# Kernel optimization log

Hardware: AMD Instinct MI355X
Metric: run time of the kernel (lower is better)

The kernel has to match this reference:

```python
import jax, jax.numpy as jnp
import numpy as np

D_MODEL = 1024
D_K = 64
D_V = 64
N_HEADS = 16
B, S = 2, 2048


def setup_inputs() -> dict:
    key = jax.random.key(0)
    ks = jax.random.split(key, 12)
    scale = 1.0 / np.sqrt(D_MODEL)
    inp = {
        "Q": jax.random.normal(ks[0], (B, S, D_MODEL), jnp.float32),
        "K": jax.random.normal(ks[1], (B, S, D_MODEL), jnp.float32),
        "V": jax.random.normal(ks[2], (B, S, D_MODEL), jnp.float32),
        # per-head projection weights (stacked over heads) and biases
        "Wq": jax.random.normal(ks[3], (N_HEADS, D_MODEL, D_K), jnp.float32) * scale,
        "bq": jax.random.normal(ks[4], (N_HEADS, D_K), jnp.float32) * 0.01,
        "Wk": jax.random.normal(ks[5], (N_HEADS, D_MODEL, D_K), jnp.float32) * scale,
        "bk": jax.random.normal(ks[6], (N_HEADS, D_K), jnp.float32) * 0.01,
        "Wv": jax.random.normal(ks[7], (N_HEADS, D_MODEL, D_V), jnp.float32) * scale,
        "bv": jax.random.normal(ks[8], (N_HEADS, D_V), jnp.float32) * 0.01,
        # output projection: (n_heads*d_v) -> d_model
        "Wo": jax.random.normal(ks[9], (N_HEADS * D_V, D_MODEL), jnp.float32) / np.sqrt(N_HEADS * D_V),
        "bo": jax.random.normal(ks[10], (D_MODEL,), jnp.float32) * 0.01,
    }
    return inp


def reference(Q, K, V, Wq, bq, Wk, bk, Wv, bv, Wo, bo):
    # Per-head projections, vectorized over heads: [B,H,S,dk]
    QW = jnp.einsum("bsd,hdk->bhsk", Q, Wq) + bq[None, :, None, :]
    KW = jnp.einsum("bsd,hdk->bhsk", K, Wk) + bk[None, :, None, :]
    VW = jnp.einsum("bsd,hdv->bhsv", V, Wv) + bv[None, :, None, :]
    # scores: [B,H,S,S]
    scores = jnp.einsum("bhsk,bhtk->bhst", QW, KW)
    # Faithful to torch source: softmax FIRST, then divide by d_k, then by 2
    attn = jax.nn.softmax(scores, axis=-1) / D_K / 2.0
    ctx = jnp.einsum("bhst,bhtv->bhsv", attn, VW)  # [B,H,S,dv]
    # concat heads along last dim (head order == torch concat order)
    ctx = jnp.transpose(ctx, (0, 2, 1, 3)).reshape(B, S, N_HEADS * D_V)
    return ctx @ Wo + bo
```

## Files before the change

kernel.cpp:

```cpp
#include <hip/hip_runtime.h>

typedef unsigned short u16;
typedef unsigned int u32;
typedef __attribute__((ext_vector_type(8))) short bf16x8;
typedef __attribute__((ext_vector_type(4))) float f32x4;

__device__ __forceinline__ u16 f2b(float f) {
    union { float f; u32 u; } v; v.f = f;
    return (u16)((v.u + 0x7FFF + ((v.u >> 16) & 1)) >> 16);
}

__device__ __forceinline__ void glds16(const u16* g, u16* l) {
    __builtin_amdgcn_global_load_lds(
        (const __attribute__((address_space(1))) void*)g,
        (__attribute__((address_space(3))) void*)l, 16, 0, 0);
}

__global__ __launch_bounds__(256) void cast3(
    const float* __restrict__ Q, const float* __restrict__ K,
    const float* __restrict__ V,
    u16* __restrict__ Qb, u16* __restrict__ Kb, u16* __restrict__ Vb)
{
    const float* in = (blockIdx.z == 0) ? Q : (blockIdx.z == 1) ? K : V;
    u16* out = (blockIdx.z == 0) ? Qb : (blockIdx.z == 1) ? Kb : Vb;
    const int n4 = 1048576;
    const int stride = gridDim.x * 256;
    for (int i = blockIdx.x * 256 + threadIdx.x; i < n4; i += stride) {
        float4 v = ((const float4*)in)[i];
        ushort4 o;
        o.x = f2b(v.x); o.y = f2b(v.y); o.z = f2b(v.z); o.w = f2b(v.w);
        ((ushort4*)out)[i] = o;
    }
}

__global__ __launch_bounds__(256) void tcastW(
    const float* __restrict__ Wq, const float* __restrict__ Wk,
    const float* __restrict__ Wv,
    u16* __restrict__ WqT, u16* __restrict__ WkT, u16* __restrict__ WvT)
{
    __shared__ float t[64][68];
    const int sel = blockIdx.z >> 4, hz = blockIdx.z & 15;
    const float* in = (sel == 0) ? Wq : (sel == 1) ? Wk : Wv;
    u16* out = (sel == 0) ? WqT : (sel == 1) ? WkT : WvT;
    const long mb = (long)hz * 65536;
    const int r0 = blockIdx.x * 64;
    const int tid = threadIdx.x;
    const int rr = tid >> 4, c4 = (tid & 15) * 4;

    #pragma unroll
    for (int p = 0; p < 4; ++p) {
        float4 v = *(const float4*)(in + mb + (long)(r0 + p * 16 + rr) * 64 + c4);
        *(float4*)&t[p * 16 + rr][c4] = v;
    }
    __syncthreads();
    #pragma unroll
    for (int p = 0; p < 4; ++p) {
        const int oc = p * 16 + rr;
        const int r4 = (tid & 15) * 4;
        ushort4 o;
        o.x = f2b(t[r4 + 0][oc]); o.y = f2b(t[r4 + 1][oc]);
        o.z = f2b(t[r4 + 2][oc]); o.w = f2b(t[r4 + 3][oc]);
        *(ushort4*)(out + mb + (long)oc * 1024 + r0 + r4) = o;
    }
}

__global__ __launch_bounds__(256) void tcastWo(
    const float* __restrict__ in, u16* __restrict__ out)
{
    __shared__ float t[64][68];
    const int r0 = blockIdx.x * 64, c0 = blockIdx.y * 64;
    const int tid = threadIdx.x;
    const int rr = tid >> 4, c4 = (tid & 15) * 4;

    #pragma unroll
    for (int p = 0; p < 4; ++p) {
        float4 v = *(const float4*)(in + (long)(r0 + p * 16 + rr) * 1024 + c0 + c4);
        *(float4*)&t[p * 16 + rr][c4] = v;
    }
    __syncthreads();
    #pragma unroll
    for (int p = 0; p < 4; ++p) {
        const int oc = p * 16 + rr;
        const int r4 = (tid & 15) * 4;
        ushort4 o;
        o.x = f2b(t[r4 + 0][oc]); o.y = f2b(t[r4 + 1][oc]);
        o.z = f2b(t[r4 + 2][oc]); o.w = f2b(t[r4 + 3][oc]);
        *(ushort4*)(out + (long)(c0 + oc) * 1024 + r0 + r4) = o;
    }
}

#define GEMM_CORE(A_, BT_)                                                     \
    __shared__ u16 As[128 * 64];                                               \
    __shared__ u16 Bs[128 * 64];                                               \
    const int tid = threadIdx.x, lane = tid & 63, w = tid >> 6;                \
    const int m0 = blockIdx.y * 128, n0 = blockIdx.x * 128;                    \
    const int wm = (w >> 1) * 64, wn = (w & 1) * 64;                           \
    const int fr = lane & 15, quad = lane >> 4;                                \
    f32x4 acc[4][4];                                                           \
    const f32x4 zero = {0.f, 0.f, 0.f, 0.f};                                   \
    _Pragma("unroll")                                                          \
    for (int mi = 0; mi < 4; ++mi)                                             \
        _Pragma("unroll")                                                      \
        for (int ni = 0; ni < 4; ++ni) acc[mi][ni] = zero;                     \
    const int srow = lane >> 3;                                                \
    const int schk = (lane & 7) ^ (srow & 7);       \
    const long ga = (long)(m0 + srow) * 1024 + schk * 8;                       \
    const long gb = (long)(n0 + srow) * 1024 + schk * 8;                       \
    const int f7 = fr & 7;                                                     \
    for (int k0 = 0; k0 < 1024; k0 += 64) {                                    \
        __syncthreads();                                                       \
        _Pragma("unroll")                                                      \
        for (int i2 = 0; i2 < 4; ++i2) {                                       \
            const int i = w * 4 + i2;                                          \
            glds16(A_ + ga + (long)i * 8 * 1024 + k0, &As[i * 512]);           \
            glds16(BT_ + gb + (long)i * 8 * 1024 + k0, &Bs[i * 512]);          \
        }                                                                      \
        __syncthreads();                                                       \
        _Pragma("unroll")                                                      \
        for (int kc = 0; kc < 2; ++kc) {                                       \
            const int pos = ((kc * 4 + quad) ^ f7) * 8;                        \
            bf16x8 af[4], bfr[4];                                              \
            _Pragma("unroll")                                                  \
            for (int mi = 0; mi < 4; ++mi)                                     \
                af[mi] = *(const bf16x8*)&As[(wm + mi * 16 + fr) * 64 + pos];  \
            _Pragma("unroll")                                                  \
            for (int ni = 0; ni < 4; ++ni)                                     \
                bfr[ni] = *(const bf16x8*)&Bs[(wn + ni * 16 + fr) * 64 + pos]; \
            _Pragma("unroll")                                                  \
            for (int mi = 0; mi < 4; ++mi)                                     \
                _Pragma("unroll")                                              \
                for (int ni = 0; ni < 4; ++ni)                                 \
                    acc[mi][ni] = __builtin_amdgcn_mfma_f32_16x16x32_bf16(     \
                        af[mi], bfr[ni], acc[mi][ni], 0, 0, 0);                \
        }                                                                      \
    }

__global__ __launch_bounds__(256) void proj3(
    const u16* __restrict__ Qb, const u16* __restrict__ Kb,
    const u16* __restrict__ Vb,
    const u16* __restrict__ WqT, const u16* __restrict__ WkT,
    const u16* __restrict__ WvT,
    const float* __restrict__ bq, const float* __restrict__ bk,
    const float* __restrict__ bv,
    u16* __restrict__ QWb, u16* __restrict__ KWb, u16* __restrict__ VWb)
{
    const int z = blockIdx.z;
    const u16* A  = (z == 0) ? Qb : (z == 1) ? Kb : Vb;
    const u16* BT = (z == 0) ? WqT : (z == 1) ? WkT : WvT;
    const float* bias = (z == 0) ? bq : (z == 1) ? bk : bv;
    u16* Cu = (z == 0) ? QWb : (z == 1) ? KWb : VWb;

    GEMM_CORE(A, BT)

    #pragma unroll
    for (int mi = 0; mi < 4; ++mi) {
        #pragma unroll
        for (int ni = 0; ni < 4; ++ni) {
            #pragma unroll
            for (int r = 0; r < 4; ++r) {
                const int m = m0 + wm + mi * 16 + quad * 4 + r;
                const int c = n0 + wn + ni * 16 + fr;
                const float v = acc[mi][ni][r] + bias[c];
                const int b = m >> 11, s = m & 2047, h = c >> 6, k = c & 63;
                if (z != 2)
                    Cu[((long)(b * 16 + h) * 2048 + s) * 64 + k] = f2b(v);
                else
                    Cu[((long)(b * 16 + h) * 64 + k) * 2048 + s] = f2b(v);
            }
        }
    }
}

__global__ __launch_bounds__(256) void gemm_out(
    const u16* __restrict__ A, const u16* __restrict__ BT,
    const float* __restrict__ bias, float* __restrict__ Cf)
{
    GEMM_CORE(A, BT)

    #pragma unroll
    for (int mi = 0; mi < 4; ++mi) {
        #pragma unroll
        for (int ni = 0; ni < 4; ++ni) {
            #pragma unroll
            for (int r = 0; r < 4; ++r) {
                const int m = m0 + wm + mi * 16 + quad * 4 + r;
                const int c = n0 + wn + ni * 16 + fr;
                Cf[(long)m * 1024 + c] = acc[mi][ni][r] + bias[c];
            }
        }
    }
}

__global__ __launch_bounds__(256) void attn_mfma(
    const u16* __restrict__ QW, const u16* __restrict__ KW,
    const u16* __restrict__ VW, u16* __restrict__ ctxb)
{
    __shared__ u16 kt[64 * 64];
    __shared__ u16 vt[64 * 64];
    __shared__ u16 ps[4][32 * 72];

    const int tid = threadIdx.x, lane = tid & 63, w = tid >> 6;
    const int bh = blockIdx.y, b = bh >> 4, h = bh & 15;
    const int q0 = blockIdx.x * 128;
    const int fr = lane & 15, quad = lane >> 4;
    const int f7 = fr & 7;

    bf16x8 aQ[2][2];
    #pragma unroll
    for (int s = 0; s < 2; ++s) {
        const u16* qp = QW + ((long)bh * 2048 + q0 + w * 32 + s * 16 + fr) * 64;
        aQ[s][0] = *(const bf16x8*)(qp + quad * 8);
        aQ[s][1] = *(const bf16x8*)(qp + 32 + quad * 8);
    }

    const f32x4 zero = {0.f, 0.f, 0.f, 0.f};
    f32x4 acc[2][4], lac[2];
    #pragma unroll
    for (int s = 0; s < 2; ++s) {
        lac[s] = zero;
        #pragma unroll
        for (int d = 0; d < 4; ++d) acc[s][d] = zero;
    }
    bf16x8 bones;
    #pragma unroll
    for (int j = 0; j < 8; ++j) bones[j] = (short)0x3F80;

    const int srow = lane >> 3;
    const int schk = (lane & 7) ^ (srow & 7);
    const long kgb = (long)bh * (2048 * 64);
    const long vgb = (long)bh * (64 * 2048);

    for (int t0 = 0; t0 < 2048; t0 += 64) {
        __syncthreads();
        #pragma unroll
        for (int i2 = 0; i2 < 2; ++i2) {
            const int i = w * 2 + i2;
            glds16(KW + kgb + (long)(t0 + i * 8 + srow) * 64 + schk * 8, &kt[i * 512]);
            glds16(VW + vgb + (long)(i * 8 + srow) * 2048 + t0 + schk * 8, &vt[i * 512]);
        }
        __syncthreads();

        const int pos0 = (quad ^ f7) * 8;
        const int pos1 = pos0 ^ 32;

        #pragma unroll
        for (int s = 0; s < 2; ++s) {
            f32x4 sc[4];
            #pragma unroll
            for (int sub = 0; sub < 4; ++sub) {
                const int row = (sub * 16 + fr) * 64;
                bf16x8 b0 = *(const bf16x8*)&kt[row + pos0];
                bf16x8 b1 = *(const bf16x8*)&kt[row + pos1];
                f32x4 z = __builtin_amdgcn_mfma_f32_16x16x32_bf16(aQ[s][0], b0, zero, 0, 0, 0);
                sc[sub]  = __builtin_amdgcn_mfma_f32_16x16x32_bf16(aQ[s][1], b1, z, 0, 0, 0);
            }
            u16* pw = ps[w] + s * 16 * 72;
            #pragma unroll
            for (int sub = 0; sub < 4; ++sub)
                #pragma unroll
                for (int r = 0; r < 4; ++r)
                    pw[(quad * 4 + r) * 72 + sub * 16 + fr] = f2b(__expf(sc[sub][r]));
        }
        __asm__ volatile("s_waitcnt lgkmcnt(0)" ::: "memory");

        #pragma unroll
        for (int s = 0; s < 2; ++s) {
            const u16* pw = ps[w] + s * 16 * 72;
            const bf16x8 aP0 = *(const bf16x8*)&pw[fr * 72 + quad * 8];
            const bf16x8 aP1 = *(const bf16x8*)&pw[fr * 72 + 32 + quad * 8];
            lac[s] = __builtin_amdgcn_mfma_f32_16x16x32_bf16(aP0, bones, lac[s], 0, 0, 0);
            lac[s] = __builtin_amdgcn_mfma_f32_16x16x32_bf16(aP1, bones, lac[s], 0, 0, 0);
            #pragma unroll
            for (int d = 0; d < 4; ++d) {
                const int row = (d * 16 + fr) * 64;
                bf16x8 v0 = *(const bf16x8*)&vt[row + pos0];
                bf16x8 v1 = *(const bf16x8*)&vt[row + pos1];
                acc[s][d] = __builtin_amdgcn_mfma_f32_16x16x32_bf16(aP0, v0, acc[s][d], 0, 0, 0);
                acc[s][d] = __builtin_amdgcn_mfma_f32_16x16x32_bf16(aP1, v1, acc[s][d], 0, 0, 0);
            }
        }
    }

    #pragma unroll
    for (int s = 0; s < 2; ++s) {
        #pragma unroll
        for (int r = 0; r < 4; ++r) {
            const float scl = 1.0f / (lac[s][r] * 128.0f);
            const long row = (long)b * 2048 + q0 + w * 32 + s * 16 + quad * 4 + r;
            #pragma unroll
            for (int d = 0; d < 4; ++d)
                ctxb[row * 1024 + h * 64 + d * 16 + fr] = f2b(acc[s][d][r] * scl);
        }
    }
}

extern "C" void kernel_launch(void* const* d_in, const int* in_sizes, int n_in,
                              void* d_out, int out_size, void* d_ws, size_t ws_size,
                              hipStream_t stream) {
    (void)in_sizes; (void)n_in; (void)out_size; (void)ws_size;

    const float* Q  = (const float*)d_in[0];
    const float* K  = (const float*)d_in[1];
    const float* V  = (const float*)d_in[2];
    const float* Wq = (const float*)d_in[3];
    const float* bq = (const float*)d_in[4];
    const float* Wk = (const float*)d_in[5];
    const float* bk = (const float*)d_in[6];
    const float* Wv = (const float*)d_in[7];
    const float* bv = (const float*)d_in[8];
    const float* Wo = (const float*)d_in[9];
    const float* bo = (const float*)d_in[10];
    float* out = (float*)d_out;

    u16* ws  = (u16*)d_ws;
    u16* Qb  = ws;
    u16* Kb  = Qb  + 4194304;
    u16* Vb  = Kb  + 4194304;
    u16* WqT = Vb  + 4194304;
    u16* WkT = WqT + 1048576;
    u16* WvT = WkT + 1048576;
    u16* WoT = WvT + 1048576;
    u16* QWb = WoT + 1048576;
    u16* KWb = QWb + 4194304;
    u16* VWb = KWb + 4194304;
    u16* ctx = VWb + 4194304;

    cast3<<<dim3(1024, 1, 3), 256, 0, stream>>>(Q, K, V, Qb, Kb, Vb);
    tcastW<<<dim3(16, 1, 48), 256, 0, stream>>>(Wq, Wk, Wv, WqT, WkT, WvT);
    tcastWo<<<dim3(16, 16), 256, 0, stream>>>(Wo, WoT);

    proj3<<<dim3(8, 32, 3), 256, 0, stream>>>(Qb, Kb, Vb, WqT, WkT, WvT,
                                              bq, bk, bv, QWb, KWb, VWb);

    attn_mfma<<<dim3(16, 32), 256, 0, stream>>>(QWb, KWb, VWb, ctx);

    gemm_out<<<dim3(8, 32), 256, 0, stream>>>(ctx, WoT, bo, out);
}
```

Measured before the change: 265.3 us.

## Double-buffer K/V tiles in attention and halve queries per block

The attention kernel now double-buffers the K and V tiles in LDS. The next tile's global-to-LDS loads are issued before computing on the current one, and only one barrier is kept per iteration. Each block handles 64 queries instead of 128, which doubles the grid and halves per-wave accumulator registers. The QK MFMA operands are swapped so scores come out transposed, so P can be stored with packed bf16 conversions and wider LDS writes, and s_setprio is raised around the MFMA sections. In exchange, each K/V tile is reused by fewer queries, so K/V load traffic doubles, and LDS use grows.

```diff
diff --git a/kernel.cpp b/kernel.cpp
--- a/kernel.cpp
+++ b/kernel.cpp
@@ -195,32 +195,24 @@
     const u16* __restrict__ QW, const u16* __restrict__ KW,
     const u16* __restrict__ VW, u16* __restrict__ ctxb)
 {
-    __shared__ u16 kt[64 * 64];
-    __shared__ u16 vt[64 * 64];
-    __shared__ u16 ps[4][32 * 72];
+    __shared__ u16 kt[2][64 * 64];
+    __shared__ u16 vt[2][64 * 64];
+    __shared__ u16 ps[4][16 * 72];
 
     const int tid = threadIdx.x, lane = tid & 63, w = tid >> 6;
     const int bh = blockIdx.y, b = bh >> 4, h = bh & 15;
-    const int q0 = blockIdx.x * 128;
+    const int q0 = blockIdx.x * 64;
     const int fr = lane & 15, quad = lane >> 4;
     const int f7 = fr & 7;
 
-    bf16x8 aQ[2][2];
-    #pragma unroll
-    for (int s = 0; s < 2; ++s) {
-        const u16* qp = QW + ((long)bh * 2048 + q0 + w * 32 + s * 16 + fr) * 64;
-        aQ[s][0] = *(const bf16x8*)(qp + quad * 8);
-        aQ[s][1] = *(const bf16x8*)(qp + 32 + quad * 8);
-    }
+    const u16* qp = QW + ((long)bh * 2048 + q0 + w * 16 + fr) * 64;
+    const bf16x8 aQ0 = *(const bf16x8*)(qp + quad * 8);
+    const bf16x8 aQ1 = *(const bf16x8*)(qp + 32 + quad * 8);
 
     const f32x4 zero = {0.f, 0.f, 0.f, 0.f};
-    f32x4 acc[2][4], lac[2];
-    #pragma unroll
-    for (int s = 0; s < 2; ++s) {
-        lac[s] = zero;
-        #pragma unroll
-        for (int d = 0; d < 4; ++d) acc[s][d] = zero;
-    }
+    f32x4 acc[4], lac = zero;
+    #pragma unroll
+    for (int d = 0; d < 4; ++d) acc[d] = zero;
     bf16x8 bones;
     #pragma unroll
     for (int j = 0; j < 8; ++j) bones[j] = (short)0x3F80;
@@ -230,67 +222,80 @@
     const long kgb = (long)bh * (2048 * 64);
     const long vgb = (long)bh * (64 * 2048);
 
+#define ATTN_STAGE(p_, t_)                                                    \
+    _Pragma("unroll")                                                         \
+    for (int i2 = 0; i2 < 2; ++i2) {                                          \
+        const int i = w * 2 + i2;                                             \
+        glds16(KW + kgb + (long)((t_) + i * 8 + srow) * 64 + schk * 8,        \
+               &kt[p_][i * 512]);                                             \
+        glds16(VW + vgb + (long)(i * 8 + srow) * 2048 + (t_) + schk * 8,      \
+               &vt[p_][i * 512]);                                             \
+    }
+
+    ATTN_STAGE(0, 0)
+    __syncthreads();
+
+    const int pos0 = (quad ^ f7) * 8;
+    const int pos1 = pos0 ^ 32;
+    u16* pw = ps[w];
+
     for (int t0 = 0; t0 < 2048; t0 += 64) {
+        const int p = (t0 >> 6) & 1;
+        if (t0 + 64 < 2048) { ATTN_STAGE(p ^ 1, t0 + 64) }
+
+        const u16* ktp = kt[p];
+        const u16* vtp = vt[p];
+
+        f32x4 sc[4];
+        __builtin_amdgcn_s_setprio(1);
+        #pragma unroll
+        for (int sub = 0; sub < 4; ++sub) {
+            const int row = (sub * 16 + fr) * 64;
+            bf16x8 k0 = *(const bf16x8*)&ktp[row + pos0];
+            bf16x8 k1 = *(const bf16x8*)&ktp[row + pos1];
+            f32x4 z = __builtin_amdgcn_mfma_f32_16x16x32_bf16(k0, aQ0, zero, 0, 0, 0);
+            sc[sub]  = __builtin_amdgcn_mfma_f32_16x16x32_bf16(k1, aQ1, z, 0, 0, 0);
+        }
+        __builtin_amdgcn_s_setprio(0);
+
+        #pragma unroll
+        for (int sub = 0; sub < 4; ++sub) {
+            float e0 = __expf(sc[sub][0]);
+            float e1 = __expf(sc[sub][1]);
+            float e2 = __expf(sc[sub][2]);
+            float e3 = __expf(sc[sub][3]);
+            u32 lo, hi;
+            asm("v_cvt_pk_bf16_f32 %0, %1, %2" : "=v"(lo) : "v"(e0), "v"(e1));
+            asm("v_cvt_pk_bf16_f32 %0, %1, %2" : "=v"(hi) : "v"(e2), "v"(e3));
+            uint2 pk2; pk2.x = lo; pk2.y = hi;
+            *(uint2*)&pw[fr * 72 + sub * 16 + quad * 4] = pk2;
+        }
+        __asm__ volatile("s_waitcnt lgkmcnt(0)" ::: "memory");
+
+        const bf16x8 aP0 = *(const bf16x8*)&pw[fr * 72 + quad * 8];
+        const bf16x8 aP1 = *(const bf16x8*)&pw[fr * 72 + 32 + quad * 8];
+        __builtin_amdgcn_s_setprio(1);
+        lac = __builtin_amdgcn_mfma_f32_16x16x32_bf16(aP0, bones, lac, 0, 0, 0);
+        lac = __builtin_amdgcn_mfma_f32_16x16x32_bf16(aP1, bones, lac, 0, 0, 0);
+        #pragma unroll
+        for (int d = 0; d < 4; ++d) {
+            const int row = (d * 16 + fr) * 64;
+            bf16x8 v0 = *(const bf16x8*)&vtp[row + pos0];
+            bf16x8 v1 = *(const bf16x8*)&vtp[row + pos1];
+            acc[d] = __builtin_amdgcn_mfma_f32_16x16x32_bf16(aP0, v0, acc[d], 0, 0, 0);
+            acc[d] = __builtin_amdgcn_mfma_f32_16x16x32_bf16(aP1, v1, acc[d], 0, 0, 0);
+        }
+        __builtin_amdgcn_s_setprio(0);
         __syncthreads();
-        #pragma unroll
-        for (int i2 = 0; i2 < 2; ++i2) {
-            const int i = w * 2 + i2;
-            glds16(KW + kgb + (long)(t0 + i * 8 + srow) * 64 + schk * 8, &kt[i * 512]);
-            glds16(VW + vgb + (long)(i * 8 + srow) * 2048 + t0 + schk * 8, &vt[i * 512]);
-        }
-        __syncthreads();
-
-        const int pos0 = (quad ^ f7) * 8;
-        const int pos1 = pos0 ^ 32;
-
-        #pragma unroll
-        for (int s = 0; s < 2; ++s) {
-            f32x4 sc[4];
-            #pragma unroll
-            for (int sub = 0; sub < 4; ++sub) {
-                const int row = (sub * 16 + fr) * 64;
-                bf16x8 b0 = *(const bf16x8*)&kt[row + pos0];
-                bf16x8 b1 = *(const bf16x8*)&kt[row + pos1];
-                f32x4 z = __builtin_amdgcn_mfma_f32_16x16x32_bf16(aQ[s][0], b0, zero, 0, 0, 0);
-                sc[sub]  = __builtin_amdgcn_mfma_f32_16x16x32_bf16(aQ[s][1], b1, z, 0, 0, 0);
-            }
-            u16* pw = ps[w] + s * 16 * 72;
-            #pragma unroll
-            for (int sub = 0; sub < 4; ++sub)
-                #pragma unroll
-                for (int r = 0; r < 4; ++r)
-                    pw[(quad * 4 + r) * 72 + sub * 16 + fr] = f2b(__expf(sc[sub][r]));
-        }
-        __asm__ volatile("s_waitcnt lgkmcnt(0)" ::: "memory");
-
-        #pragma unroll
-        for (int s = 0; s < 2; ++s) {
-            const u16* pw = ps[w] + s * 16 * 72;
-            const bf16x8 aP0 = *(const bf16x8*)&pw[fr * 72 + quad * 8];
-            const bf16x8 aP1 = *(const bf16x8*)&pw[fr * 72 + 32 + quad * 8];
-            lac[s] = __builtin_amdgcn_mfma_f32_16x16x32_bf16(aP0, bones, lac[s], 0, 0, 0);
-            lac[s] = __builtin_amdgcn_mfma_f32_16x16x32_bf16(aP1, bones, lac[s], 0, 0, 0);
-            #pragma unroll
-            for (int d = 0; d < 4; ++d) {
-                const int row = (d * 16 + fr) * 64;
-                bf16x8 v0 = *(const bf16x8*)&vt[row + pos0];
-                bf16x8 v1 = *(const bf16x8*)&vt[row + pos1];
-                acc[s][d] = __builtin_amdgcn_mfma_f32_16x16x32_bf16(aP0, v0, acc[s][d], 0, 0, 0);
-                acc[s][d] = __builtin_amdgcn_mfma_f32_16x16x32_bf16(aP1, v1, acc[s][d], 0, 0, 0);
-            }
-        }
-    }
-
-    #pragma unroll
-    for (int s = 0; s < 2; ++s) {
-        #pragma unroll
-        for (int r = 0; r < 4; ++r) {
-            const float scl = 1.0f / (lac[s][r] * 128.0f);
-            const long row = (long)b * 2048 + q0 + w * 32 + s * 16 + quad * 4 + r;
-            #pragma unroll
-            for (int d = 0; d < 4; ++d)
-                ctxb[row * 1024 + h * 64 + d * 16 + fr] = f2b(acc[s][d][r] * scl);
-        }
+    }
+
+    #pragma unroll
+    for (int r = 0; r < 4; ++r) {
+        const float scl = 1.0f / (lac[r] * 128.0f);
+        const long row = (long)b * 2048 + q0 + w * 16 + quad * 4 + r;
+        #pragma unroll
+        for (int d = 0; d < 4; ++d)
+            ctxb[row * 1024 + h * 64 + d * 16 + fr] = f2b(acc[d][r] * scl);
     }
 }
 
@@ -332,7 +337,7 @@
     proj3<<<dim3(8, 32, 3), 256, 0, stream>>>(Qb, Kb, Vb, WqT, WkT, WvT,
                                               bq, bk, bv, QWb, KWb, VWb);
 
-    attn_mfma<<<dim3(16, 32), 256, 0, stream>>>(QWb, KWb, VWb, ctx);
+    attn_mfma<<<dim3(32, 32), 256, 0, stream>>>(QWb, KWb, VWb, ctx);
 
     gemm_out<<<dim3(8, 32), 256, 0, stream>>>(ctx, WoT, bo, out);
 }
```

After: 276.9 us. 1.04x slower.

## Double-buffer K/V tiles in attention and pack exp outputs with cvt_pk_bf16

Applied to the files above, without the earlier changes.

Adds two LDS buffers for K and V tiles so the next tile's global-to-LDS loads are issued before the current tile is computed, which removes one barrier per iteration and overlaps load latency with compute. The QK^T MFMA swaps its operands so the score layout is transposed, which lets the four exp values be packed with v_cvt_pk_bf16_f32 and written as a single 8-byte LDS store instead of scalar u16 stores. s_setprio brackets the MFMA sections. LDS use grows by 16KB per block, which may reduce occupancy.

```diff
diff --git a/kernel.cpp b/kernel.cpp
--- a/kernel.cpp
+++ b/kernel.cpp
@@ -195,8 +195,8 @@
     const u16* __restrict__ QW, const u16* __restrict__ KW,
     const u16* __restrict__ VW, u16* __restrict__ ctxb)
 {
-    __shared__ u16 kt[64 * 64];
-    __shared__ u16 vt[64 * 64];
+    __shared__ u16 kt[2][64 * 64];
+    __shared__ u16 vt[2][64 * 64];
     __shared__ u16 ps[4][32 * 72];
 
     const int tid = threadIdx.x, lane = tid & 63, w = tid >> 6;
@@ -230,55 +230,80 @@
     const long kgb = (long)bh * (2048 * 64);
     const long vgb = (long)bh * (64 * 2048);
 
+#define ATTN_STAGE(p_, t_)                                                    \
+    _Pragma("unroll")                                                         \
+    for (int i2 = 0; i2 < 2; ++i2) {                                          \
+        const int i = w * 2 + i2;                                             \
+        glds16(KW + kgb + (long)((t_) + i * 8 + srow) * 64 + schk * 8,        \
+               &kt[p_][i * 512]);                                             \
+        glds16(VW + vgb + (long)(i * 8 + srow) * 2048 + (t_) + schk * 8,      \
+               &vt[p_][i * 512]);                                             \
+    }
+
+    ATTN_STAGE(0, 0)
+    __syncthreads();
+
+    const int pos0 = (quad ^ f7) * 8;
+    const int pos1 = pos0 ^ 32;
+    u16* pw = ps[w];
+
     for (int t0 = 0; t0 < 2048; t0 += 64) {
-        __syncthreads();
-        #pragma unroll
-        for (int i2 = 0; i2 < 2; ++i2) {
-            const int i = w * 2 + i2;
-            glds16(KW + kgb + (long)(t0 + i * 8 + srow) * 64 + schk * 8, &kt[i * 512]);
-            glds16(VW + vgb + (long)(i * 8 + srow) * 2048 + t0 + schk * 8, &vt[i * 512]);
-        }
-        __syncthreads();
-
-        const int pos0 = (quad ^ f7) * 8;
-        const int pos1 = pos0 ^ 32;
-
+        const int p = (t0 >> 6) & 1;
+        if (t0 + 64 < 2048) { ATTN_STAGE(p ^ 1, t0 + 64) }
+
+        const u16* ktp = kt[p];
+        const u16* vtp = vt[p];
+
+        f32x4 sc[2][4];
+        __builtin_amdgcn_s_setprio(1);
         #pragma unroll
         for (int s = 0; s < 2; ++s) {
-            f32x4 sc[4];
             #pragma unroll
             for (int sub = 0; sub < 4; ++sub) {
                 const int row = (sub * 16 + fr) * 64;
-                bf16x8 b0 = *(const bf16x8*)&kt[row + pos0];
-                bf16x8 b1 = *(const bf16x8*)&kt[row + pos1];
-                f32x4 z = __builtin_amdgcn_mfma_f32_16x16x32_bf16(aQ[s][0], b0, zero, 0, 0, 0);
-                sc[sub]  = __builtin_amdgcn_mfma_f32_16x16x32_bf16(aQ[s][1], b1, z, 0, 0, 0);
-            }
-            u16* pw = ps[w] + s * 16 * 72;
-            #pragma unroll
-            for (int sub = 0; sub < 4; ++sub)
-                #pragma unroll
-                for (int r = 0; r < 4; ++r)
-                    pw[(quad * 4 + r) * 72 + sub * 16 + fr] = f2b(__expf(sc[sub][r]));
+                bf16x8 k0 = *(const bf16x8*)&ktp[row + pos0];
+                bf16x8 k1 = *(const bf16x8*)&ktp[row + pos1];
+                f32x4 z = __builtin_amdgcn_mfma_f32_16x16x32_bf16(k0, aQ[s][0], zero, 0, 0, 0);
+                sc[s][sub] = __builtin_amdgcn_mfma_f32_16x16x32_bf16(k1, aQ[s][1], z, 0, 0, 0);
+            }
+        }
+        __builtin_amdgcn_s_setprio(0);
+
+        #pragma unroll
+        for (int s = 0; s < 2; ++s) {
+            #pragma unroll
+            for (int sub = 0; sub < 4; ++sub) {
+                float e0 = __expf(sc[s][sub][0]);
+                float e1 = __expf(sc[s][sub][1]);
+                float e2 = __expf(sc[s][sub][2]);
+                float e3 = __expf(sc[s][sub][3]);
+                u32 lo, hi;
+                asm("v_cvt_pk_bf16_f32 %0, %1, %2" : "=v"(lo) : "v"(e0), "v"(e1));
+                asm("v_cvt_pk_bf16_f32 %0, %1, %2" : "=v"(hi) : "v"(e2), "v"(e3));
+                uint2 pk2; pk2.x = lo; pk2.y = hi;
+                *(uint2*)&pw[(s * 16 + fr) * 72 + sub * 16 + quad * 4] = pk2;
+            }
         }
         __asm__ volatile("s_waitcnt lgkmcnt(0)" ::: "memory");
 
+        __builtin_amdgcn_s_setprio(1);
         #pragma unroll
         for (int s = 0; s < 2; ++s) {
-            const u16* pw = ps[w] + s * 16 * 72;
-            const bf16x8 aP0 = *(const bf16x8*)&pw[fr * 72 + quad * 8];
-            const bf16x8 aP1 = *(const bf16x8*)&pw[fr * 72 + 32 + quad * 8];
+            const bf16x8 aP0 = *(const bf16x8*)&pw[(s * 16 + fr) * 72 + quad * 8];
+            const bf16x8 aP1 = *(const bf16x8*)&pw[(s * 16 + fr) * 72 + 32 + quad * 8];
             lac[s] = __builtin_amdgcn_mfma_f32_16x16x32_bf16(aP0, bones, lac[s], 0, 0, 0);
             lac[s] = __builtin_amdgcn_mfma_f32_16x16x32_bf16(aP1, bones, lac[s], 0, 0, 0);
             #pragma unroll
             for (int d = 0; d < 4; ++d) {
                 const int row = (d * 16 + fr) * 64;
-                bf16x8 v0 = *(const bf16x8*)&vt[row + pos0];
-                bf16x8 v1 = *(const bf16x8*)&vt[row + pos1];
+                bf16x8 v0 = *(const bf16x8*)&vtp[row + pos0];
+                bf16x8 v1 = *(const bf16x8*)&vtp[row + pos1];
                 acc[s][d] = __builtin_amdgcn_mfma_f32_16x16x32_bf16(aP0, v0, acc[s][d], 0, 0, 0);
                 acc[s][d] = __builtin_amdgcn_mfma_f32_16x16x32_bf16(aP1, v1, acc[s][d], 0, 0, 0);
             }
         }
+        __builtin_amdgcn_s_setprio(0);
+        __syncthreads();
     }
 
     #pragma unroll
```

Result: faster. 250.2 us (-5.7%).
